# Performance work log

Hardware: AMD Instinct MI355X
Metric: run time of the kernel (lower is better)

Reference implementation:

```python
import jax, jax.numpy as jnp
import numpy as np

D_IN = 1024
D_OUT = 1024
NUM_HEADS = 16
HEAD_DIM = D_OUT // NUM_HEADS


def setup_inputs() -> dict:
    key = jax.random.key(0)
    kx, kq, kk, kv = jax.random.split(key, 4)
    x = jax.random.normal(kx, (2, 2048, D_IN), dtype=jnp.float32)
    W_q = jax.random.normal(kq, (D_IN, D_OUT), dtype=jnp.float32)
    W_k = jax.random.normal(kk, (D_IN, D_OUT), dtype=jnp.float32)
    W_v = jax.random.normal(kv, (D_IN, D_OUT), dtype=jnp.float32)
    return {"x": x, "W_q": W_q, "W_k": W_k, "W_v": W_v}


def reference(x, W_q, W_k, W_v):
    B, S, _ = x.shape
    H, Dh = NUM_HEADS, HEAD_DIM
    # project and split heads -> [B, H, S, Dh]
    q = (x @ W_q).reshape(B, S, H, Dh).transpose(0, 2, 1, 3)
    k = (x @ W_k).reshape(B, S, H, Dh).transpose(0, 2, 1, 3)
    v = (x @ W_v).reshape(B, S, H, Dh).transpose(0, 2, 1, 3)
    scores = jnp.einsum('bhqd,bhkd->bhqk', q, k) / jnp.sqrt(jnp.float32(Dh))
    causal = jnp.tril(jnp.ones((S, S), dtype=bool))  # True where allowed
    scores = jnp.where(causal[None, None], scores, -jnp.inf)
    weights = jax.nn.softmax(scores, axis=-1)
    ctx = jnp.einsum('bhqk,bhkd->bhqd', weights, v)
    return ctx.transpose(0, 2, 1, 3).reshape(B, S, H * Dh)
```

## Files before the change

### kernel.cpp

```cpp
#include <hip/hip_runtime.h>
#include <hip/hip_bf16.h>

#define B 2
#define S 2048
#define DIN 1024
#define DOUT 1024
#define NH 16
#define DH 64
#define M_TOT (B * S)

typedef __attribute__((ext_vector_type(8))) short bf16x8;
typedef __attribute__((ext_vector_type(8))) unsigned short u16x8;
typedef __attribute__((ext_vector_type(4))) float f32x4;
typedef __attribute__((ext_vector_type(16))) float f32x16;

#define ASTRIDE 4194304
#define WSTRIDE 1048576

__device__ __forceinline__ ushort f2bf(float x) {
    union { float f; unsigned u; } c; c.f = x;
    unsigned r = (c.u + 0x7FFFu + ((c.u >> 16) & 1u)) >> 16;
    return (ushort)r;
}
__device__ __forceinline__ float bf2f(ushort h) {
    union { unsigned u; float f; } c; c.u = ((unsigned)h) << 16;
    return c.f;
}
__device__ __forceinline__ f32x4 mfma16(bf16x8 a, bf16x8 b, f32x4 c) {
    return __builtin_amdgcn_mfma_f32_16x16x32_bf16(a, b, c, 0, 0, 0);
}
__device__ __forceinline__ f32x16 mfma32(bf16x8 a, bf16x8 b, f32x16 c) {
    return __builtin_amdgcn_mfma_f32_32x32x16_bf16(a, b, c, 0, 0, 0);
}
__device__ __forceinline__ unsigned cvt_pk(float lo, float hi) {
    unsigned r;
    asm("v_cvt_pk_bf16_f32 %0, %1, %2" : "=v"(r) : "v"(lo), "v"(hi));
    return r;
}
__device__ __forceinline__ float exp2fast(float x) {
    float r;
    asm("v_exp_f32 %0, %1" : "=v"(r) : "v"(x));
    return r;
}


__global__ __launch_bounds__(256) void split_x(const float* __restrict__ x,
                                               ushort* __restrict__ xs) {
    const size_t gid = (size_t)blockIdx.x * 256 + threadIdx.x;
    const float4 v = *reinterpret_cast<const float4*>(x + gid * 4);
    const float in[4] = {v.x, v.y, v.z, v.w};
    ushort h0[4], h1[4];
#pragma unroll
    for (int e = 0; e < 4; ++e) {
        h0[e] = f2bf(in[e]);
        h1[e] = f2bf(in[e] - bf2f(h0[e]));
    }
    const size_t o = gid * 4;
    *reinterpret_cast<ushort4*>(xs + o)           = ushort4{h0[0], h0[1], h0[2], h0[3]};
    *reinterpret_cast<ushort4*>(xs + ASTRIDE + o) = ushort4{h1[0], h1[1], h1[2], h1[3]};
}

__global__ __launch_bounds__(256) void split_wT3(const float* __restrict__ W0,
                                                 const float* __restrict__ W1,
                                                 const float* __restrict__ W2,
                                                 ushort* __restrict__ wt) {
    __shared__ float Ws[64][68];
    const int tid = threadIdx.x;
    const int k0 = blockIdx.x << 6;
    const int n0 = blockIdx.y << 6;
    const int wi = blockIdx.z;
    const float* W = (wi == 0) ? W0 : (wi == 1) ? W1 : W2;
    ushort* wto = wt + (size_t)wi * 2 * WSTRIDE;

    const int r = tid >> 2;
    const int cb = (tid & 3) << 2;
#pragma unroll
    for (int it = 0; it < 4; ++it) {
        const int c = cb + (it << 4);
        *reinterpret_cast<float4*>(&Ws[r][c]) =
            *reinterpret_cast<const float4*>(&W[(size_t)(k0 + r) * 1024 + n0 + c]);
    }
    __syncthreads();
    const int rn = tid >> 2;
    const int kc = (tid & 3) << 4;
    u16x8 o0[2], o1[2];
#pragma unroll
    for (int half = 0; half < 2; ++half)
#pragma unroll
        for (int i = 0; i < 8; ++i) {
            const float x = Ws[kc + (half << 3) + i][rn];
            const ushort a = f2bf(x);
            o0[half][i] = a;
            o1[half][i] = f2bf(x - bf2f(a));
        }
    const size_t base = (size_t)(n0 + rn) * 1024 + k0 + kc;
    *reinterpret_cast<u16x8*>(wto + base)               = o0[0];
    *reinterpret_cast<u16x8*>(wto + base + 8)           = o0[1];
    *reinterpret_cast<u16x8*>(wto + WSTRIDE + base)     = o1[0];
    *reinterpret_cast<u16x8*>(wto + WSTRIDE + base + 8) = o1[1];
}

__global__ __launch_bounds__(256, 2) void proj_fused5(const ushort* __restrict__ xsp,
                                                      const ushort* __restrict__ wtsp,
                                                      float* __restrict__ qf,
                                                      ushort* __restrict__ ksp,
                                                      ushort* __restrict__ vtsp) {
    __shared__ __align__(16) ushort SL[36864];

    const int tid = threadIdx.x;
    const int lane = tid & 63;
    const int w = tid >> 6;
    const int swz = (blockIdx.x & 7) * 64 + (blockIdx.x >> 3);
    const int n0 = (swz & 15) << 6;
    const int m0 = (swz >> 4) << 7;
    const int col = lane & 15;
    const int glane = lane >> 4;
    const int lrow = lane >> 3;
    const int sl8 = ((lane & 7) ^ lrow) << 3;

    f32x4 accq[2][4], acck[2][4], accv[2][4];
#pragma unroll
    for (int mi = 0; mi < 2; ++mi)
#pragma unroll
        for (int nj = 0; nj < 4; ++nj) {
            accq[mi][nj] = f32x4{0.f, 0.f, 0.f, 0.f};
            acck[mi][nj] = f32x4{0.f, 0.f, 0.f, 0.f};
            accv[mi][nj] = f32x4{0.f, 0.f, 0.f, 0.f};
        }

    for (int k0 = 0; k0 < DIN; k0 += 64) {
        __syncthreads();
#pragma unroll
        for (int i = 0; i < 18; ++i) {
            const int u = (i << 2) | w;
            const ushort* g;
            if (u < 32) {
                const int sp = u >> 4, rb = u & 15;
                g = xsp + (size_t)sp * ASTRIDE + (size_t)(m0 + (rb << 3) + lrow) * 1024 + k0 + sl8;
            } else {
                const int v = u - 32;
                const int bi = v >> 3;
                const int rb = v & 7;
                g = wtsp + (size_t)bi * WSTRIDE + (size_t)(n0 + (rb << 3) + lrow) * 1024 + k0 + sl8;
            }
            __builtin_amdgcn_global_load_lds(g, &SL[u * 512], 16, 0, 0);
        }
        __syncthreads();

#pragma unroll
        for (int st = 0; st < 2; ++st) {
            const int sw = (((st << 2) | glane) ^ (col & 7)) << 3;
            bf16x8 a[2][2];
#pragma unroll
            for (int sp = 0; sp < 2; ++sp)
#pragma unroll
                for (int mi = 0; mi < 2; ++mi) {
                    const int arow = (w << 5) + (mi << 4) + col;
                    a[sp][mi] = *reinterpret_cast<const bf16x8*>(&SL[sp * 8192 + arow * 64 + sw]);
                }
#pragma unroll
            for (int nj = 0; nj < 4; ++nj) {
                const int brow = (nj << 4) + col;
                const int bb = 16384 + brow * 64 + sw;
                const bf16x8 bq0 = *reinterpret_cast<const bf16x8*>(&SL[bb]);
                const bf16x8 bq1 = *reinterpret_cast<const bf16x8*>(&SL[bb + 4096]);
                const bf16x8 bk0 = *reinterpret_cast<const bf16x8*>(&SL[bb + 8192]);
                const bf16x8 bk1 = *reinterpret_cast<const bf16x8*>(&SL[bb + 12288]);
                const bf16x8 bv0 = *reinterpret_cast<const bf16x8*>(&SL[bb + 16384]);
#pragma unroll
                for (int mi = 0; mi < 2; ++mi) {
                    accq[mi][nj] = mfma16(a[0][mi], bq0, accq[mi][nj]);
                    accq[mi][nj] = mfma16(a[1][mi], bq0, accq[mi][nj]);
                    accq[mi][nj] = mfma16(a[0][mi], bq1, accq[mi][nj]);
                    acck[mi][nj] = mfma16(a[0][mi], bk0, acck[mi][nj]);
                    acck[mi][nj] = mfma16(a[1][mi], bk0, acck[mi][nj]);
                    acck[mi][nj] = mfma16(a[0][mi], bk1, acck[mi][nj]);
                    accv[mi][nj] = mfma16(bv0, a[0][mi], accv[mi][nj]);
                    accv[mi][nj] = mfma16(bv0, a[1][mi], accv[mi][nj]);
                }
            }
        }
    }

    const int b = m0 >> 11;
    const int h = n0 >> 6;
    const size_t bh_off = (size_t)(b * NH + h) * S * DH;
#pragma unroll
    for (int mi = 0; mi < 2; ++mi)
#pragma unroll
        for (int r = 0; r < 4; ++r) {
            const int srow = (m0 & (S - 1)) + (w << 5) + (mi << 4) + (glane << 2) + r;
#pragma unroll
            for (int nj = 0; nj < 4; ++nj) {
                const size_t o = bh_off + (size_t)srow * DH + (nj << 4) + col;
                qf[o] = accq[mi][nj][r];
                const float xk = acck[mi][nj][r];
                const ushort k0s = f2bf(xk);
                ksp[o] = k0s;
                ksp[ASTRIDE + o] = f2bf(xk - bf2f(k0s));
            }
        }

    const int cm = col >> 2;
    const int colp = (col & 3) | ((((cm & 1) << 1) | (cm >> 1)) << 2);
    const size_t vbh = (size_t)(b * NH + h) * DH * S;
#pragma unroll
    for (int mi = 0; mi < 2; ++mi) {
        const int s = (m0 & (S - 1)) + (w << 5) + (mi << 4) + colp;
#pragma unroll
        for (int nj = 0; nj < 4; ++nj)
#pragma unroll
            for (int r = 0; r < 4; ++r) {
                const int d = (nj << 4) + (glane << 2) + r;
                vtsp[vbh + (size_t)d * S + s] = f2bf(accv[mi][nj][r]);
            }
    }
}

__global__ __launch_bounds__(128, 2) void attn_mfma8(const float* __restrict__ Qf,
                                                     const ushort* __restrict__ ksp,
                                                     const ushort* __restrict__ vtsp,
                                                     float* __restrict__ out) {
    __shared__ __align__(16) ushort KL[2][4096];
    __shared__ __align__(16) ushort VL[4096];

    const int tid = threadIdx.x;
    const int lane = tid & 63;
    const int w = tid >> 6;

    const int xcd = blockIdx.x & 7;
    const int u_ = blockIdx.x >> 3;
    const int s_ = u_ & 31, p_ = u_ >> 5;
    const int bh = (xcd << 2) | ((s_ >> 4) << 1) | (p_ >> 1);
    const int j_ = s_ & 15;
    const int qt = (p_ & 1) ? (16 + j_) : (15 - j_);

    const int q0 = qt << 6;
    const int qw0 = q0 + (w << 5);
    const int hi = lane >> 5;
    const int ql = lane & 31;
    const int qg = qw0 + ql;
    const int lrow = lane >> 3;
    const int sl8 = ((lane & 7) ^ lrow) << 3;

    bf16x8 qb[2][4];
    {
        const float* qp = Qf + ((size_t)bh * S + qg) * DH + (hi << 3);
#pragma unroll
        for (int dc = 0; dc < 4; ++dc) {
            const float4 f0 = *reinterpret_cast<const float4*>(qp + (dc << 4));
            const float4 f1 = *reinterpret_cast<const float4*>(qp + (dc << 4) + 4);
            const float xs[8] = {f0.x, f0.y, f0.z, f0.w, f1.x, f1.y, f1.z, f1.w};
#pragma unroll
            for (int e = 0; e < 8; ++e) {
                const float x = xs[e] * 0.18033688011112042f;
                const ushort h0 = f2bf(x);
                qb[0][dc][e] = (short)h0;
                qb[1][dc][e] = (short)f2bf(x - bf2f(h0));
            }
        }
    }

    f32x16 O[2];
#pragma unroll
    for (int ds = 0; ds < 2; ++ds)
#pragma unroll
        for (int r = 0; r < 16; ++r) O[ds][r] = 0.f;
    float m_ = -INFINITY, l_ = 0.f;

    const size_t kbase = (size_t)bh * S * DH;
    const size_t vbase = (size_t)bh * DH * S;

#define ISSUE_K(K0)                                                                     \
    {                                                                                   \
        _Pragma("unroll")                                                               \
        for (int i = 0; i < 8; ++i) {                                                   \
            const int u = (i << 1) | w;                                                 \
            const int sp = u >> 3, rb = u & 7;                                          \
            const ushort* gp = ksp + (size_t)sp * ASTRIDE + kbase +                     \
                               (size_t)((K0) + (rb << 3) + lrow) * DH + sl8;            \
            __builtin_amdgcn_global_load_lds(gp, &KL[sp][rb << 9], 16, 0, 0);           \
        }                                                                               \
    }
#define ISSUE_V(K0)                                                                     \
    {                                                                                   \
        _Pragma("unroll")                                                               \
        for (int i = 0; i < 4; ++i) {                                                   \
            const int u = (i << 1) | w;                                                 \
            const ushort* gp = vtsp + vbase +                                           \
                               (size_t)((u << 3) + lrow) * S + (K0) + sl8;              \
            __builtin_amdgcn_global_load_lds(gp, &VL[u << 9], 16, 0, 0);                \
        }                                                                               \
    }

    ISSUE_K(0);
    ISSUE_V(0);
    __syncthreads();

    for (int kt = 0; kt <= qt; ++kt) {
        const int k0 = kt << 6;

        f32x16 Sf[2];
#pragma unroll
        for (int ks = 0; ks < 2; ++ks)
#pragma unroll
            for (int r = 0; r < 16; ++r) Sf[ks][r] = 0.f;
        __builtin_amdgcn_s_setprio(1);
#pragma unroll
        for (int ks = 0; ks < 2; ++ks) {
#pragma unroll
            for (int dc = 0; dc < 4; ++dc) {
                const int row = (ks << 5) + ql;
                const int eo = row * 64 + ((((dc << 1) | hi) ^ (row & 7)) << 3);
                const bf16x8 ka = *reinterpret_cast<const bf16x8*>(&KL[0][eo]);
                const bf16x8 kb = *reinterpret_cast<const bf16x8*>(&KL[1][eo]);
                Sf[ks] = mfma32(ka, qb[0][dc], Sf[ks]);
                Sf[ks] = mfma32(ka, qb[1][dc], Sf[ks]);
                Sf[ks] = mfma32(kb, qb[0][dc], Sf[ks]);
                Sf[ks] = mfma32(kb, qb[1][dc], Sf[ks]);
            }
        }
        __builtin_amdgcn_s_setprio(0);

        __syncthreads();
        if (kt < qt) ISSUE_K(k0 + 64);

        if (k0 + 63 > qw0) {
#pragma unroll
            for (int ks = 0; ks < 2; ++ks)
#pragma unroll
                for (int r = 0; r < 16; ++r) {
                    const int kg = k0 + (ks << 5) + (r & 3) + ((r >> 2) << 3) + (hi << 2);
                    if (kg > qg) Sf[ks][r] = -1e30f;
                }
        }

        float mx[8];
#pragma unroll
        for (int i = 0; i < 8; ++i)
            mx[i] = fmaxf(fmaxf(Sf[0][i], Sf[0][i + 8]),
                          fmaxf(Sf[1][i], Sf[1][i + 8]));
        float rm = fmaxf(fmaxf(fmaxf(mx[0], mx[1]), fmaxf(mx[2], mx[3])),
                         fmaxf(fmaxf(mx[4], mx[5]), fmaxf(mx[6], mx[7])));
        rm = fmaxf(rm, __shfl_xor(rm, 32));
        if (__any(rm > m_ + 8.f)) {
            const float nm = fmaxf(m_, rm);
            const float sc = exp2fast(m_ - nm);
            m_ = nm;
            l_ *= sc;
#pragma unroll
            for (int ds = 0; ds < 2; ++ds)
#pragma unroll
                for (int r = 0; r < 16; ++r) O[ds][r] *= sc;
        }

        float rsa[4] = {0.f, 0.f, 0.f, 0.f};
        bf16x8 pb[4];
#pragma unroll
        for (int ks = 0; ks < 2; ++ks) {
            float p[16];
#pragma unroll
            for (int r = 0; r < 16; ++r) {
                p[r] = exp2fast(Sf[ks][r] - m_);
                rsa[r & 3] += p[r];
            }
#pragma unroll
            for (int c = 0; c < 2; ++c) {
                union { unsigned u[4]; bf16x8 v; } pw;
                pw.u[0] = cvt_pk(p[(c << 3) + 0], p[(c << 3) + 1]);
                pw.u[1] = cvt_pk(p[(c << 3) + 2], p[(c << 3) + 3]);
                pw.u[2] = cvt_pk(p[(c << 3) + 4], p[(c << 3) + 5]);
                pw.u[3] = cvt_pk(p[(c << 3) + 6], p[(c << 3) + 7]);
                pb[(ks << 1) + c] = pw.v;
            }
        }
        float rs = (rsa[0] + rsa[1]) + (rsa[2] + rsa[3]);
        rs += __shfl_xor(rs, 32);
        l_ += rs;

        __builtin_amdgcn_s_setprio(1);
#pragma unroll
        for (int ds = 0; ds < 2; ++ds)
#pragma unroll
            for (int kc = 0; kc < 4; ++kc) {
                const int row = (ds << 5) + ql;
                const int eo = row * 64 + ((((kc << 1) | hi) ^ (row & 7)) << 3);
                const bf16x8 va = *reinterpret_cast<const bf16x8*>(&VL[eo]);
                O[ds] = mfma32(va, pb[kc], O[ds]);
            }
        __builtin_amdgcn_s_setprio(0);

        __syncthreads();
        if (kt < qt) ISSUE_V(k0 + 64);
    }

    const float inv = 1.f / l_;
    const int b = bh >> 4, h = bh & (NH - 1);
    float* op = out + ((size_t)(b * S + qg)) * DOUT + h * DH;
#pragma unroll
    for (int ds = 0; ds < 2; ++ds)
#pragma unroll
        for (int rg = 0; rg < 4; ++rg) {
            float4 v;
            v.x = O[ds][(rg << 2) + 0] * inv;
            v.y = O[ds][(rg << 2) + 1] * inv;
            v.z = O[ds][(rg << 2) + 2] * inv;
            v.w = O[ds][(rg << 2) + 3] * inv;
            *reinterpret_cast<float4*>(&op[(ds << 5) + (rg << 3) + (hi << 2)]) = v;
        }
#undef ISSUE_K
#undef ISSUE_V
}

__global__ __launch_bounds__(256) void proj_f32(const float* __restrict__ A,
                                                const float* __restrict__ W,
                                                float* __restrict__ outf) {
    __shared__ float As[16][68];
    __shared__ float Bs[16][68];
    const int tid = threadIdx.x;
    const int m0 = blockIdx.x * 64;
    const int n0 = blockIdx.y * 64;
    const int tm = tid >> 4, tn = tid & 15;
    const int la_r = tid >> 2, la_c = (tid & 3) << 2;
    const int lb_r = tid >> 4, lb_c = (tid & 15) << 2;

    float acc[4][4];
#pragma unroll
    for (int i = 0; i < 4; ++i)
#pragma unroll
        for (int j = 0; j < 4; ++j) acc[i][j] = 0.f;

    for (int k0 = 0; k0 < DIN; k0 += 16) {
        const float4 av = *reinterpret_cast<const float4*>(&A[(size_t)(m0 + la_r) * DIN + k0 + la_c]);
        const float4 bv = *reinterpret_cast<const float4*>(&W[(size_t)(k0 + lb_r) * DOUT + n0 + lb_c]);
        __syncthreads();
        As[la_c + 0][la_r] = av.x; As[la_c + 1][la_r] = av.y;
        As[la_c + 2][la_r] = av.z; As[la_c + 3][la_r] = av.w;
        *reinterpret_cast<float4*>(&Bs[lb_r][lb_c]) = bv;
        __syncthreads();
#pragma unroll
        for (int kk = 0; kk < 16; ++kk) {
            const float4 a = *reinterpret_cast<const float4*>(&As[kk][tm << 2]);
            const float4 b = *reinterpret_cast<const float4*>(&Bs[kk][tn << 2]);
            const float aa[4] = {a.x, a.y, a.z, a.w};
            const float bb[4] = {b.x, b.y, b.z, b.w};
#pragma unroll
            for (int i = 0; i < 4; ++i)
#pragma unroll
                for (int j = 0; j < 4; ++j) acc[i][j] += aa[i] * bb[j];
        }
    }
    const int b = m0 >> 11;
    const int s_base = (m0 & (S - 1)) + (tm << 2);
    const int h = n0 >> 6;
    const int dh = tn << 2;
    float* obase = outf + ((size_t)(b * NH + h) * S) * DH;
#pragma unroll
    for (int i = 0; i < 4; ++i) {
        float4 v;
        v.x = acc[i][0]; v.y = acc[i][1]; v.z = acc[i][2]; v.w = acc[i][3];
        *reinterpret_cast<float4*>(&obase[(size_t)(s_base + i) * DH + dh]) = v;
    }
}

__global__ __launch_bounds__(256) void attn_f32(const float* __restrict__ Q,
                                                const float* __restrict__ K,
                                                const float* __restrict__ V,
                                                float* __restrict__ out) {
    __shared__ float Qs[64][68];
    __shared__ float Ks[64][68];
    __shared__ float Vs[64][68];
    __shared__ float Ps[64][68];
    const int tid = threadIdx.x;
    const int bh = blockIdx.x & 31;
    const int qt = 31 - (blockIdx.x >> 5);
    const int q0 = qt << 6;
    const int tq = tid >> 4, tk = tid & 15;
    const int sr = tid >> 2, sc = (tid & 3) << 2;

    const float* qbase = Q + ((size_t)bh * S + q0) * DH;
    const float* kbase = K + (size_t)bh * S * DH;
    const float* vbase = V + (size_t)bh * S * DH;
#pragma unroll
    for (int it = 0; it < 4; ++it) {
        const int d0 = sc + (it << 4);
        const float4 v = *reinterpret_cast<const float4*>(&qbase[(size_t)sr * DH + d0]);
        Qs[d0 + 0][sr] = v.x; Qs[d0 + 1][sr] = v.y;
        Qs[d0 + 2][sr] = v.z; Qs[d0 + 3][sr] = v.w;
    }
    float C[4][4];
#pragma unroll
    for (int i = 0; i < 4; ++i)
#pragma unroll
        for (int j = 0; j < 4; ++j) C[i][j] = 0.f;
    float m[4] = {-1e30f, -1e30f, -1e30f, -1e30f};
    float l[4] = {0.f, 0.f, 0.f, 0.f};

    for (int kt = 0; kt <= qt; ++kt) {
        const int k0 = kt << 6;
        float4 kv[4], vv[4];
#pragma unroll
        for (int it = 0; it < 4; ++it) {
            const int d0 = sc + (it << 4);
            kv[it] = *reinterpret_cast<const float4*>(&kbase[(size_t)(k0 + sr) * DH + d0]);
            vv[it] = *reinterpret_cast<const float4*>(&vbase[(size_t)(k0 + sr) * DH + d0]);
        }
        __syncthreads();
#pragma unroll
        for (int it = 0; it < 4; ++it) {
            const int d0 = sc + (it << 4);
            Ks[d0 + 0][sr] = kv[it].x; Ks[d0 + 1][sr] = kv[it].y;
            Ks[d0 + 2][sr] = kv[it].z; Ks[d0 + 3][sr] = kv[it].w;
            *reinterpret_cast<float4*>(&Vs[sr][d0]) = vv[it];
        }
        __syncthreads();

        float s[4][4];
#pragma unroll
        for (int i = 0; i < 4; ++i)
#pragma unroll
            for (int j = 0; j < 4; ++j) s[i][j] = 0.f;
#pragma unroll 16
        for (int d = 0; d < 64; ++d) {
            const float4 qf4 = *reinterpret_cast<const float4*>(&Qs[d][tq << 2]);
            const float4 kf4 = *reinterpret_cast<const float4*>(&Ks[d][tk << 2]);
            const float qa[4] = {qf4.x, qf4.y, qf4.z, qf4.w};
            const float ka[4] = {kf4.x, kf4.y, kf4.z, kf4.w};
#pragma unroll
            for (int i = 0; i < 4; ++i)
#pragma unroll
                for (int j = 0; j < 4; ++j) s[i][j] += qa[i] * ka[j];
        }
        if (kt == qt) {
#pragma unroll
            for (int i = 0; i < 4; ++i) {
                const int qg = q0 + (tq << 2) + i;
#pragma unroll
                for (int j = 0; j < 4; ++j) {
                    const int kg = k0 + (tk << 2) + j;
                    s[i][j] = (kg <= qg) ? s[i][j] * 0.125f : -1e30f;
                }
            }
        } else {
#pragma unroll
            for (int i = 0; i < 4; ++i)
#pragma unroll
                for (int j = 0; j < 4; ++j) s[i][j] *= 0.125f;
        }
#pragma unroll
        for (int i = 0; i < 4; ++i) {
            float rm = fmaxf(fmaxf(s[i][0], s[i][1]), fmaxf(s[i][2], s[i][3]));
#pragma unroll
            for (int off = 1; off < 16; off <<= 1) rm = fmaxf(rm, __shfl_xor(rm, off));
            const float mn = fmaxf(m[i], rm);
            const float scale = __expf(m[i] - mn);
            float rs = 0.f;
#pragma unroll
            for (int j = 0; j < 4; ++j) {
                s[i][j] = __expf(s[i][j] - mn);
                rs += s[i][j];
            }
#pragma unroll
            for (int off = 1; off < 16; off <<= 1) rs += __shfl_xor(rs, off);
            l[i] = l[i] * scale + rs;
            m[i] = mn;
#pragma unroll
            for (int j = 0; j < 4; ++j) C[i][j] *= scale;
            *reinterpret_cast<float4*>(&Ps[(tq << 2) + i][tk << 2]) =
                make_float4(s[i][0], s[i][1], s[i][2], s[i][3]);
        }
        __syncthreads();
#pragma unroll 4
        for (int kc = 0; kc < 16; ++kc) {
            float4 pf[4], vf[4];
#pragma unroll
            for (int i = 0; i < 4; ++i)
                pf[i] = *reinterpret_cast<const float4*>(&Ps[(tq << 2) + i][kc << 2]);
#pragma unroll
            for (int j = 0; j < 4; ++j)
                vf[j] = *reinterpret_cast<const float4*>(&Vs[(kc << 2) + j][tk << 2]);
#pragma unroll
            for (int i = 0; i < 4; ++i) {
                const float pa[4] = {pf[i].x, pf[i].y, pf[i].z, pf[i].w};
#pragma unroll
                for (int j = 0; j < 4; ++j) {
                    C[i][j] += pa[0] * ((const float*)&vf[0])[j]
                             + pa[1] * ((const float*)&vf[1])[j]
                             + pa[2] * ((const float*)&vf[2])[j]
                             + pa[3] * ((const float*)&vf[3])[j];
                }
            }
        }
        __syncthreads();
    }
    const int b = bh >> 4, h = bh & (NH - 1);
#pragma unroll
    for (int i = 0; i < 4; ++i) {
        const int qg = q0 + (tq << 2) + i;
        const float inv = 1.f / l[i];
        float4 v;
        v.x = C[i][0] * inv; v.y = C[i][1] * inv;
        v.z = C[i][2] * inv; v.w = C[i][3] * inv;
        *reinterpret_cast<float4*>(&out[((size_t)(b * S + qg)) * DOUT + h * DH + (tk << 2)]) = v;
    }
}

extern "C" void kernel_launch(void* const* d_in, const int* in_sizes, int n_in,
                              void* d_out, int out_size, void* d_ws, size_t ws_size,
                              hipStream_t stream) {
    const float* x  = (const float*)d_in[0];
    const float* Wq = (const float*)d_in[1];
    const float* Wk = (const float*)d_in[2];
    const float* Wv = (const float*)d_in[3];
    float* out = (float*)d_out;

    char* ws = (char*)d_ws;
    const size_t MB = 1024 * 1024;

    if (ws_size >= 68 * MB) {
        ushort* wtsp = (ushort*)(ws);
        ushort* xsp  = (ushort*)(ws + 12 * MB);
        float*  qf   = (float*)(ws + 28 * MB);
        ushort* ksp  = (ushort*)(ws + 44 * MB);
        ushort* vtsp = (ushort*)(ws + 60 * MB);

        split_x<<<4096, 256, 0, stream>>>(x, xsp);
        split_wT3<<<dim3(16, 16, 3), 256, 0, stream>>>(Wq, Wk, Wv, wtsp);
        proj_fused5<<<512, 256, 0, stream>>>(xsp, wtsp, qf, ksp, vtsp);
        attn_mfma8<<<1024, 128, 0, stream>>>(qf, ksp, vtsp, out);
    } else {
        float* qws = (float*)d_ws;
        float* kws = qws + (size_t)M_TOT * DOUT;
        float* vws = kws + (size_t)M_TOT * DOUT;
        dim3 pgrid(M_TOT / 64, DOUT / 64);
        proj_f32<<<pgrid, 256, 0, stream>>>(x, Wq, qws);
        proj_f32<<<pgrid, 256, 0, stream>>>(x, Wk, kws);
        proj_f32<<<pgrid, 256, 0, stream>>>(x, Wv, vws);
        attn_f32<<<32 * 32, 256, 0, stream>>>(qws, kws, vws, out);
    }
}
```

Measured before the change: 129.8 us.

## Split KV range across two wave pairs per block and merge softmax partials

Each attention block now runs four waves instead of two. The two wave pairs take disjoint halves of the causal KV tile range, each with its own LDS K/V buffer. At the end they combine their partial max, sum and output accumulators through LDS before one pair writes the result. This shortens the serial KV loop for long causal rows and raises wave-level parallelism, at the cost of more LDS per block, a merge step, and idle iterations in the shorter half. The QK product also drops the low-by-low split-bf16 MFMA term, cutting matrix work for a small precision loss.

```diff
diff --git a/kernel.cpp b/kernel.cpp
--- a/kernel.cpp
+++ b/kernel.cpp
@@ -217,16 +217,17 @@
     }
 }
 
-__global__ __launch_bounds__(128, 2) void attn_mfma8(const float* __restrict__ Qf,
+__global__ __launch_bounds__(256, 3) void attn_mfma9(const float* __restrict__ Qf,
                                                      const ushort* __restrict__ ksp,
                                                      const ushort* __restrict__ vtsp,
                                                      float* __restrict__ out) {
-    __shared__ __align__(16) ushort KL[2][4096];
-    __shared__ __align__(16) ushort VL[4096];
+    __shared__ __align__(16) ushort SB[2][12288];
 
     const int tid = threadIdx.x;
     const int lane = tid & 63;
     const int w = tid >> 6;
+    const int p = w & 1;
+    const int hf = w >> 1;
 
     const int xcd = blockIdx.x & 7;
     const int u_ = blockIdx.x >> 3;
@@ -236,13 +237,17 @@
     const int qt = (p_ & 1) ? (16 + j_) : (15 - j_);
 
     const int q0 = qt << 6;
-    const int qw0 = q0 + (w << 5);
+    const int qw0 = q0 + (p << 5);
     const int hi = lane >> 5;
     const int ql = lane & 31;
     const int qg = qw0 + ql;
     const int lrow = lane >> 3;
     const int sl8 = ((lane & 7) ^ lrow) << 3;
 
+    const int hA = (qt + 2) >> 1;
+    const int nT = hf ? (qt + 1 - hA) : hA;
+    const int tbase = hf ? hA : 0;
+
     bf16x8 qb[2][4];
     {
         const float* qp = Qf + ((size_t)bh * S + qg) * DH + (hi << 3);
@@ -270,144 +275,171 @@
 
     const size_t kbase = (size_t)bh * S * DH;
     const size_t vbase = (size_t)bh * DH * S;
+    const int wl = p;
 
 #define ISSUE_K(K0)                                                                     \
     {                                                                                   \
         _Pragma("unroll")                                                               \
         for (int i = 0; i < 8; ++i) {                                                   \
-            const int u = (i << 1) | w;                                                 \
+            const int u = (i << 1) | wl;                                                \
             const int sp = u >> 3, rb = u & 7;                                          \
             const ushort* gp = ksp + (size_t)sp * ASTRIDE + kbase +                     \
                                (size_t)((K0) + (rb << 3) + lrow) * DH + sl8;            \
-            __builtin_amdgcn_global_load_lds(gp, &KL[sp][rb << 9], 16, 0, 0);           \
+            __builtin_amdgcn_global_load_lds(gp, &SB[hf][sp * 4096 + (rb << 9)], 16, 0, 0); \
         }                                                                               \
     }
 #define ISSUE_V(K0)                                                                     \
     {                                                                                   \
         _Pragma("unroll")                                                               \
         for (int i = 0; i < 4; ++i) {                                                   \
-            const int u = (i << 1) | w;                                                 \
+            const int u = (i << 1) | wl;                                                \
             const ushort* gp = vtsp + vbase +                                           \
                                (size_t)((u << 3) + lrow) * S + (K0) + sl8;              \
-            __builtin_amdgcn_global_load_lds(gp, &VL[u << 9], 16, 0, 0);                \
+            __builtin_amdgcn_global_load_lds(gp, &SB[hf][8192 + (u << 9)], 16, 0, 0);   \
         }                                                                               \
     }
 
-    ISSUE_K(0);
-    ISSUE_V(0);
+    if (nT > 0) { ISSUE_K(tbase << 6); ISSUE_V(tbase << 6); }
     __syncthreads();
 
-    for (int kt = 0; kt <= qt; ++kt) {
-        const int k0 = kt << 6;
+    for (int kt = 0; kt < hA; ++kt) {
+        const bool act = kt < nT;
+        const int k0 = (tbase + kt) << 6;
 
         f32x16 Sf[2];
-#pragma unroll
-        for (int ks = 0; ks < 2; ++ks)
-#pragma unroll
-            for (int r = 0; r < 16; ++r) Sf[ks][r] = 0.f;
-        __builtin_amdgcn_s_setprio(1);
-#pragma unroll
-        for (int ks = 0; ks < 2; ++ks) {
-#pragma unroll
-            for (int dc = 0; dc < 4; ++dc) {
-                const int row = (ks << 5) + ql;
-                const int eo = row * 64 + ((((dc << 1) | hi) ^ (row & 7)) << 3);
-                const bf16x8 ka = *reinterpret_cast<const bf16x8*>(&KL[0][eo]);
-                const bf16x8 kb = *reinterpret_cast<const bf16x8*>(&KL[1][eo]);
-                Sf[ks] = mfma32(ka, qb[0][dc], Sf[ks]);
-                Sf[ks] = mfma32(ka, qb[1][dc], Sf[ks]);
-                Sf[ks] = mfma32(kb, qb[0][dc], Sf[ks]);
-                Sf[ks] = mfma32(kb, qb[1][dc], Sf[ks]);
-            }
-        }
-        __builtin_amdgcn_s_setprio(0);
-
-        __syncthreads();
-        if (kt < qt) ISSUE_K(k0 + 64);
-
-        if (k0 + 63 > qw0) {
+        if (act) {
 #pragma unroll
             for (int ks = 0; ks < 2; ++ks)
 #pragma unroll
+                for (int r = 0; r < 16; ++r) Sf[ks][r] = 0.f;
+            __builtin_amdgcn_s_setprio(1);
+#pragma unroll
+            for (int ks = 0; ks < 2; ++ks) {
+#pragma unroll
+                for (int dc = 0; dc < 4; ++dc) {
+                    const int row = (ks << 5) + ql;
+                    const int eo = row * 64 + ((((dc << 1) | hi) ^ (row & 7)) << 3);
+                    const bf16x8 ka = *reinterpret_cast<const bf16x8*>(&SB[hf][eo]);
+                    const bf16x8 kb = *reinterpret_cast<const bf16x8*>(&SB[hf][4096 + eo]);
+                    Sf[ks] = mfma32(ka, qb[0][dc], Sf[ks]);
+                    Sf[ks] = mfma32(ka, qb[1][dc], Sf[ks]);
+                    Sf[ks] = mfma32(kb, qb[0][dc], Sf[ks]);
+                }
+            }
+            __builtin_amdgcn_s_setprio(0);
+        }
+
+        __syncthreads();
+        if (kt + 1 < nT) ISSUE_K(k0 + 64);
+
+        if (act) {
+            if (k0 + 63 > qw0) {
+#pragma unroll
+                for (int ks = 0; ks < 2; ++ks)
+#pragma unroll
+                    for (int r = 0; r < 16; ++r) {
+                        const int kg = k0 + (ks << 5) + (r & 3) + ((r >> 2) << 3) + (hi << 2);
+                        if (kg > qg) Sf[ks][r] = -1e30f;
+                    }
+            }
+
+            float mx[8];
+#pragma unroll
+            for (int i = 0; i < 8; ++i)
+                mx[i] = fmaxf(fmaxf(Sf[0][i], Sf[0][i + 8]),
+                              fmaxf(Sf[1][i], Sf[1][i + 8]));
+            float rm = fmaxf(fmaxf(fmaxf(mx[0], mx[1]), fmaxf(mx[2], mx[3])),
+                             fmaxf(fmaxf(mx[4], mx[5]), fmaxf(mx[6], mx[7])));
+            rm = fmaxf(rm, __shfl_xor(rm, 32));
+            if (__any(rm > m_ + 8.f)) {
+                const float nm = fmaxf(m_, rm);
+                const float sc = exp2fast(m_ - nm);
+                m_ = nm;
+                l_ *= sc;
+#pragma unroll
+                for (int ds = 0; ds < 2; ++ds)
+#pragma unroll
+                    for (int r = 0; r < 16; ++r) O[ds][r] *= sc;
+            }
+
+            float rsa[4] = {0.f, 0.f, 0.f, 0.f};
+            bf16x8 pb[4];
+#pragma unroll
+            for (int ks = 0; ks < 2; ++ks) {
+                float pv[16];
+#pragma unroll
                 for (int r = 0; r < 16; ++r) {
-                    const int kg = k0 + (ks << 5) + (r & 3) + ((r >> 2) << 3) + (hi << 2);
-                    if (kg > qg) Sf[ks][r] = -1e30f;
-                }
-        }
-
-        float mx[8];
-#pragma unroll
-        for (int i = 0; i < 8; ++i)
-            mx[i] = fmaxf(fmaxf(Sf[0][i], Sf[0][i + 8]),
-                          fmaxf(Sf[1][i], Sf[1][i + 8]));
-        float rm = fmaxf(fmaxf(fmaxf(mx[0], mx[1]), fmaxf(mx[2], mx[3])),
-                         fmaxf(fmaxf(mx[4], mx[5]), fmaxf(mx[6], mx[7])));
-        rm = fmaxf(rm, __shfl_xor(rm, 32));
-        if (__any(rm > m_ + 8.f)) {
-            const float nm = fmaxf(m_, rm);
-            const float sc = exp2fast(m_ - nm);
-            m_ = nm;
-            l_ *= sc;
+                    pv[r] = exp2fast(Sf[ks][r] - m_);
+                    rsa[r & 3] += pv[r];
+                }
+#pragma unroll
+                for (int c = 0; c < 2; ++c) {
+                    union { unsigned u[4]; bf16x8 v; } pw;
+                    pw.u[0] = cvt_pk(pv[(c << 3) + 0], pv[(c << 3) + 1]);
+                    pw.u[1] = cvt_pk(pv[(c << 3) + 2], pv[(c << 3) + 3]);
+                    pw.u[2] = cvt_pk(pv[(c << 3) + 4], pv[(c << 3) + 5]);
+                    pw.u[3] = cvt_pk(pv[(c << 3) + 6], pv[(c << 3) + 7]);
+                    pb[(ks << 1) + c] = pw.v;
+                }
+            }
+            float rs = (rsa[0] + rsa[1]) + (rsa[2] + rsa[3]);
+            rs += __shfl_xor(rs, 32);
+            l_ += rs;
+
+            __builtin_amdgcn_s_setprio(1);
 #pragma unroll
             for (int ds = 0; ds < 2; ++ds)
 #pragma unroll
-                for (int r = 0; r < 16; ++r) O[ds][r] *= sc;
-        }
-
-        float rsa[4] = {0.f, 0.f, 0.f, 0.f};
-        bf16x8 pb[4];
-#pragma unroll
-        for (int ks = 0; ks < 2; ++ks) {
-            float p[16];
-#pragma unroll
-            for (int r = 0; r < 16; ++r) {
-                p[r] = exp2fast(Sf[ks][r] - m_);
-                rsa[r & 3] += p[r];
-            }
-#pragma unroll
-            for (int c = 0; c < 2; ++c) {
-                union { unsigned u[4]; bf16x8 v; } pw;
-                pw.u[0] = cvt_pk(p[(c << 3) + 0], p[(c << 3) + 1]);
-                pw.u[1] = cvt_pk(p[(c << 3) + 2], p[(c << 3) + 3]);
-                pw.u[2] = cvt_pk(p[(c << 3) + 4], p[(c << 3) + 5]);
-                pw.u[3] = cvt_pk(p[(c << 3) + 6], p[(c << 3) + 7]);
-                pb[(ks << 1) + c] = pw.v;
-            }
-        }
-        float rs = (rsa[0] + rsa[1]) + (rsa[2] + rsa[3]);
-        rs += __shfl_xor(rs, 32);
-        l_ += rs;
-
-        __builtin_amdgcn_s_setprio(1);
+                for (int kc = 0; kc < 4; ++kc) {
+                    const int row = (ds << 5) + ql;
+                    const int eo = row * 64 + ((((kc << 1) | hi) ^ (row & 7)) << 3);
+                    const bf16x8 va = *reinterpret_cast<const bf16x8*>(&SB[hf][8192 + eo]);
+                    O[ds] = mfma32(va, pb[kc], O[ds]);
+                }
+            __builtin_amdgcn_s_setprio(0);
+        }
+
+        __syncthreads();
+        if (kt + 1 < nT) ISSUE_V(k0 + 64);
+    }
+
+    float* CF = reinterpret_cast<float*>(&SB[0][0]);
+    if (hf == 1) {
 #pragma unroll
         for (int ds = 0; ds < 2; ++ds)
 #pragma unroll
-            for (int kc = 0; kc < 4; ++kc) {
-                const int row = (ds << 5) + ql;
-                const int eo = row * 64 + ((((kc << 1) | hi) ^ (row & 7)) << 3);
-                const bf16x8 va = *reinterpret_cast<const bf16x8*>(&VL[eo]);
-                O[ds] = mfma32(va, pb[kc], O[ds]);
-            }
-        __builtin_amdgcn_s_setprio(0);
-
-        __syncthreads();
-        if (kt < qt) ISSUE_V(k0 + 64);
-    }
-
-    const float inv = 1.f / l_;
-    const int b = bh >> 4, h = bh & (NH - 1);
-    float* op = out + ((size_t)(b * S + qg)) * DOUT + h * DH;
-#pragma unroll
-    for (int ds = 0; ds < 2; ++ds)
-#pragma unroll
-        for (int rg = 0; rg < 4; ++rg) {
-            float4 v;
-            v.x = O[ds][(rg << 2) + 0] * inv;
-            v.y = O[ds][(rg << 2) + 1] * inv;
-            v.z = O[ds][(rg << 2) + 2] * inv;
-            v.w = O[ds][(rg << 2) + 3] * inv;
-            *reinterpret_cast<float4*>(&op[(ds << 5) + (rg << 3) + (hi << 2)]) = v;
-        }
+            for (int r = 0; r < 16; ++r)
+                CF[((p * 2 + ds) * 16 + r) * 64 + lane] = O[ds][r];
+        if (lane < 32) {
+            CF[4096 + p * 64 + lane * 2]     = m_;
+            CF[4096 + p * 64 + lane * 2 + 1] = l_;
+        }
+    }
+    __syncthreads();
+    if (hf == 0) {
+        const float mB = CF[4096 + p * 64 + ql * 2];
+        const float lB = CF[4096 + p * 64 + ql * 2 + 1];
+        const float m = fmaxf(m_, mB);
+        const float sA = exp2fast(m_ - m);
+        const float sB = exp2fast(mB - m);
+        const float l = l_ * sA + lB * sB;
+        const float inv = 1.f / l;
+        const int b = bh >> 4, h = bh & (NH - 1);
+        float* op = out + ((size_t)(b * S + qg)) * DOUT + h * DH;
+#pragma unroll
+        for (int ds = 0; ds < 2; ++ds)
+#pragma unroll
+            for (int rg = 0; rg < 4; ++rg) {
+                float4 v;
+#pragma unroll
+                for (int e = 0; e < 4; ++e) {
+                    const int r = (rg << 2) + e;
+                    const float ob = CF[((p * 2 + ds) * 16 + r) * 64 + lane];
+                    ((float*)&v)[e] = (O[ds][r] * sA + ob * sB) * inv;
+                }
+                *reinterpret_cast<float4*>(&op[(ds << 5) + (rg << 3) + (hi << 2)]) = v;
+            }
+    }
 #undef ISSUE_K
 #undef ISSUE_V
 }
@@ -627,7 +659,7 @@
         split_x<<<4096, 256, 0, stream>>>(x, xsp);
         split_wT3<<<dim3(16, 16, 3), 256, 0, stream>>>(Wq, Wk, Wv, wtsp);
         proj_fused5<<<512, 256, 0, stream>>>(xsp, wtsp, qf, ksp, vtsp);
-        attn_mfma8<<<1024, 128, 0, stream>>>(qf, ksp, vtsp, out);
+        attn_mfma9<<<1024, 256, 0, stream>>>(qf, ksp, vtsp, out);
     } else {
         float* qws = (float*)d_ws;
         float* kws = qws + (size_t)M_TOT * DOUT;
```

After: 150.0 us. 1.16x slower.
